# Performance work log

Hardware: AMD Instinct MI355X
Metric: run time of the kernel (lower is better)

Reference implementation:

```python
import jax, jax.numpy as jnp
import numpy as np

B, C, F, J = 64, 16, 2048, 25
EMBED, CLASSES, NJ = 64, 5, 12
AFFECT = slice(0, 12)
UNAFFECT = slice(12, 24)


def setup_inputs() -> dict:
    key = jax.random.key(0)
    k0, k1, k2, k3 = jax.random.split(key, 4)
    features = jax.random.normal(k0, (B, C, F, J), dtype=jnp.float32)
    W1 = jax.random.normal(k1, (EMBED, C, NJ), dtype=jnp.float32) * 0.05
    b1 = jnp.zeros((EMBED,), jnp.float32)
    W2 = jax.random.normal(k2, (EMBED, C, NJ), dtype=jnp.float32) * 0.05
    b2 = jnp.zeros((EMBED,), jnp.float32)
    Wl = jax.random.normal(k3, (CLASSES, 16 * EMBED), dtype=jnp.float32) * 0.02
    bl = jnp.zeros((CLASSES,), jnp.float32)
    return {"features": features, "W1": W1, "b1": b1, "W2": W2, "b2": b2, "Wl": Wl, "bl": bl}


def _stat_features(x, proto):
    # x: [b, c, f, j]; single sort shared by min/max/quantiles/median
    f = x.shape[-2]
    xs = jnp.sort(x, axis=-2)

    def quant(p):
        # torch.quantile linear interpolation
        pos = p * (f - 1)
        lo = int(np.floor(pos)); hi = int(np.ceil(pos)); frac = np.float32(pos - lo)
        return xs[..., lo, :] * (1.0 - frac) + xs[..., hi, :] * frac

    s1 = xs[..., 0, :]                       # min
    s2 = xs[..., -1, :]                      # max
    s3 = quant(0.25)
    s4 = xs[..., (f - 1) // 2, :]            # torch.median: lower middle element
    s5 = quant(0.75)
    s6 = jnp.mean(x, axis=-2)
    s7 = jnp.std(x, axis=-2, ddof=1)         # torch.std unbiased
    s8 = s2 - s1
    z = (x - s6[..., None, :]) / s7[..., None, :]
    if proto:
        s9 = jnp.mean(z ** 3, axis=-2)       # skew
    else:
        s9 = jnp.mean(z ** 4, axis=-2) - 3.0  # excess kurtosis
    return jnp.stack([s2, s3, s4, s5, s6, s7, s8, s9], axis=-2)  # [b, c, 8, j]


def _fuse(stat, W, b):
    # Conv2d kernel (1, joints) == contraction over (c, j) per stat row
    out = jnp.einsum('bcsj,ecj->bes', stat, W) + b[None, :, None]
    return out.reshape(out.shape[0], -1)  # flatten (embed, stats) like torch.flatten


def reference(features, W1, b1, W2, b2, Wl, bl):
    affected = features[:, :, :, AFFECT]
    unaffected = features[:, :, :, UNAFFECT]
    stat_af = _stat_features(affected, proto=False)
    stat_ua = _stat_features(unaffected, proto=False)
    # attn=False path (STAT_VA block disabled)
    stat1 = _stat_features(unaffected + affected, proto=True)
    _ = _fuse(stat1, W1, b1)  # stat1 branch only feeds CL loss (get_cl_loss=False)
    stat2 = jnp.concatenate([stat_af, stat_ua], axis=-2)  # [b, c, 16, j]
    flat2 = _fuse(stat2, W2, b2)                          # [b, 16*embed]
    logits = flat2 @ Wl.T + bl
    return logits
```

## Files before the change

kernel.cpp:

```cpp
#include <hip/hip_runtime.h>
#include <hip/hip_bf16.h>
#include <math.h>


#define F_LEN 2048
#define JTOT 25
#define STATS_PER_BC 192
#define LP 2056

__device__ __forceinline__ int swz(int i) {
  return (i & ~31) | ((i + ((i >> 5) << 2)) & 31);
}

template <int PAT>
__device__ __forceinline__ float ds_swz(float v) {
  return __int_as_float(
      __builtin_amdgcn_ds_swizzle(__float_as_int(v), PAT));
}

template <int CTRL, int BANK>
__device__ __forceinline__ int upd_dpp(int old_, int src) {
  return __builtin_amdgcn_update_dpp(old_, src, CTRL, 0xF, BANK, false);
}

__device__ __forceinline__ float xpartner(float v, const int lm,
                                          const int addr32) {
  const int vi = __float_as_int(v);
  switch (lm) {
    case 1:  return __int_as_float(upd_dpp<0xB1, 0xF>(vi, vi));
    case 2:  return __int_as_float(upd_dpp<0x4E, 0xF>(vi, vi));
    case 4: {
      const int t1 = upd_dpp<0x104, 0x5>(vi, vi);
      const int t2 = upd_dpp<0x114, 0xA>(t1, vi);
      return __int_as_float(t2);
    }
    case 8:  return __int_as_float(upd_dpp<0x128, 0xF>(vi, vi));
    case 16: return ds_swz<0x401F>(v);
    default:
      return __int_as_float(
          __builtin_amdgcn_ds_bpermute(addr32, vi));
  }
}

__device__ __forceinline__ float wave_sum(float v, int addr32) {
  v += xpartner(v, 1, addr32);
  v += xpartner(v, 2, addr32);
  v += xpartner(v, 4, addr32);
  v += xpartner(v, 8, addr32);
  v += xpartner(v, 16, addr32);
  v += xpartner(v, 32, addr32);
  return v;
}

#define XSUB8(CTRL, a0, a1, a2, a3, a4, a5, a6, a7, FL)                       \
  do {                                                                        \
    float t0, t1, t2, t3, t4, t5, t6, t7;                                     \
    asm volatile(                                                             \
        "v_xor_b32 %0, %16, %0\n\t"                                           \
        "v_xor_b32 %1, %16, %1\n\t"                                           \
        "v_xor_b32 %2, %16, %2\n\t"                                           \
        "v_xor_b32 %3, %16, %3\n\t"                                           \
        "v_xor_b32 %4, %16, %4\n\t"                                           \
        "v_xor_b32 %5, %16, %5\n\t"                                           \
        "v_xor_b32 %6, %16, %6\n\t"                                           \
        "v_xor_b32 %7, %16, %7\n\t"                                           \
        "v_mov_b32_dpp %8, %0 " CTRL "\n\t"                                   \
        "v_mov_b32_dpp %9, %1 " CTRL "\n\t"                                   \
        "v_mov_b32_dpp %10, %2 " CTRL "\n\t"                                  \
        "v_mov_b32_dpp %11, %3 " CTRL "\n\t"                                  \
        "v_mov_b32_dpp %12, %4 " CTRL "\n\t"                                  \
        "v_mov_b32_dpp %13, %5 " CTRL "\n\t"                                  \
        "v_mov_b32_dpp %14, %6 " CTRL "\n\t"                                  \
        "v_mov_b32_dpp %15, %7 " CTRL "\n\t"                                  \
        "v_min_f32 %0, %0, -%8\n\t"                                           \
        "v_min_f32 %1, %1, -%9\n\t"                                           \
        "v_min_f32 %2, %2, -%10\n\t"                                          \
        "v_min_f32 %3, %3, -%11\n\t"                                          \
        "v_min_f32 %4, %4, -%12\n\t"                                          \
        "v_min_f32 %5, %5, -%13\n\t"                                          \
        "v_min_f32 %6, %6, -%14\n\t"                                          \
        "v_min_f32 %7, %7, -%15\n\t"                                          \
        : "+v"(a0), "+v"(a1), "+v"(a2), "+v"(a3), "+v"(a4), "+v"(a5),         \
          "+v"(a6), "+v"(a7), "=&v"(t0), "=&v"(t1), "=&v"(t2), "=&v"(t3),     \
          "=&v"(t4), "=&v"(t5), "=&v"(t6), "=&v"(t7)                          \
        : "v"(FL));                                                           \
  } while (0)

#define XSUB8_X4(a0, a1, a2, a3, a4, a5, a6, a7, FL)                          \
  do {                                                                        \
    float t0, t1, t2, t3, t4, t5, t6, t7;                                     \
    asm volatile(                                                             \
        "v_xor_b32 %0, %16, %0\n\t"                                           \
        "v_xor_b32 %1, %16, %1\n\t"                                           \
        "v_xor_b32 %2, %16, %2\n\t"                                           \
        "v_xor_b32 %3, %16, %3\n\t"                                           \
        "v_xor_b32 %4, %16, %4\n\t"                                           \
        "v_xor_b32 %5, %16, %5\n\t"                                           \
        "v_xor_b32 %6, %16, %6\n\t"                                           \
        "v_xor_b32 %7, %16, %7\n\t"                                           \
        "v_mov_b32_dpp %8, %0 row_shl:4 row_mask:0xf bank_mask:0x5\n\t"       \
        "v_mov_b32_dpp %9, %1 row_shl:4 row_mask:0xf bank_mask:0x5\n\t"       \
        "v_mov_b32_dpp %10, %2 row_shl:4 row_mask:0xf bank_mask:0x5\n\t"      \
        "v_mov_b32_dpp %11, %3 row_shl:4 row_mask:0xf bank_mask:0x5\n\t"      \
        "v_mov_b32_dpp %12, %4 row_shl:4 row_mask:0xf bank_mask:0x5\n\t"      \
        "v_mov_b32_dpp %13, %5 row_shl:4 row_mask:0xf bank_mask:0x5\n\t"      \
        "v_mov_b32_dpp %14, %6 row_shl:4 row_mask:0xf bank_mask:0x5\n\t"      \
        "v_mov_b32_dpp %15, %7 row_shl:4 row_mask:0xf bank_mask:0x5\n\t"      \
        "v_mov_b32_dpp %8, %0 row_shr:4 row_mask:0xf bank_mask:0xa\n\t"       \
        "v_mov_b32_dpp %9, %1 row_shr:4 row_mask:0xf bank_mask:0xa\n\t"       \
        "v_mov_b32_dpp %10, %2 row_shr:4 row_mask:0xf bank_mask:0xa\n\t"      \
        "v_mov_b32_dpp %11, %3 row_shr:4 row_mask:0xf bank_mask:0xa\n\t"      \
        "v_mov_b32_dpp %12, %4 row_shr:4 row_mask:0xf bank_mask:0xa\n\t"      \
        "v_mov_b32_dpp %13, %5 row_shr:4 row_mask:0xf bank_mask:0xa\n\t"      \
        "v_mov_b32_dpp %14, %6 row_shr:4 row_mask:0xf bank_mask:0xa\n\t"      \
        "v_mov_b32_dpp %15, %7 row_shr:4 row_mask:0xf bank_mask:0xa\n\t"      \
        "v_min_f32 %0, %0, -%8\n\t"                                           \
        "v_min_f32 %1, %1, -%9\n\t"                                           \
        "v_min_f32 %2, %2, -%10\n\t"                                          \
        "v_min_f32 %3, %3, -%11\n\t"                                          \
        "v_min_f32 %4, %4, -%12\n\t"                                          \
        "v_min_f32 %5, %5, -%13\n\t"                                          \
        "v_min_f32 %6, %6, -%14\n\t"                                          \
        "v_min_f32 %7, %7, -%15\n\t"                                          \
        : "+v"(a0), "+v"(a1), "+v"(a2), "+v"(a3), "+v"(a4), "+v"(a5),         \
          "+v"(a6), "+v"(a7), "=&v"(t0), "=&v"(t1), "=&v"(t2), "=&v"(t3),     \
          "=&v"(t4), "=&v"(t5), "=&v"(t6), "=&v"(t7)                          \
        : "v"(FL));                                                           \
  } while (0)

#define QP1 "quad_perm:[1,0,3,2] row_mask:0xf bank_mask:0xf"
#define QP2 "quad_perm:[2,3,0,1] row_mask:0xf bank_mask:0xf"
#define ROR8 "row_ror:8 row_mask:0xf bank_mask:0xf"

#define XSUB32(M, CTRL, X, FL)                                                \
  do {                                                                        \
    M(CTRL, X[0], X[1], X[2], X[3], X[4], X[5], X[6], X[7], FL);              \
    M(CTRL, X[8], X[9], X[10], X[11], X[12], X[13], X[14], X[15], FL);        \
    M(CTRL, X[16], X[17], X[18], X[19], X[20], X[21], X[22], X[23], FL);      \
    M(CTRL, X[24], X[25], X[26], X[27], X[28], X[29], X[30], X[31], FL);      \
  } while (0)

#define XSUB32_X4(X, FL)                                                      \
  do {                                                                        \
    XSUB8_X4(X[0], X[1], X[2], X[3], X[4], X[5], X[6], X[7], FL);             \
    XSUB8_X4(X[8], X[9], X[10], X[11], X[12], X[13], X[14], X[15], FL);       \
    XSUB8_X4(X[16], X[17], X[18], X[19], X[20], X[21], X[22], X[23], FL);     \
    XSUB8_X4(X[24], X[25], X[26], X[27], X[28], X[29], X[30], X[31], FL);     \
  } while (0)

__global__ __launch_bounds__(256) void stat_kernel(
    const float* __restrict__ Fp, float* __restrict__ stat2) {
  __shared__ float lds[4 * LP];
  const int g = blockIdx.x;
  const int xcd = g & 7;
  const int mm = g >> 3;
  const int bc = xcd * 128 + mm / 6;
  const int grp = mm % 6;
  const int t = threadIdx.x;
  const int w = t >> 6;
  const int lane = t & 63;
  const int addr32 = ((lane ^ 32) << 2);
  const int j0 = grp * 4;
  float* wlds = lds + w * LP;

  {
    const float* bbase = Fp + (size_t)bc * F_LEN * JTOT + j0;
    const int f0 = t >> 2, jj = t & 3;
    float* ldst = lds + jj * LP;
#pragma unroll
    for (int it = 0; it < 32; ++it) {
      const int f = it * 64 + f0;
      ldst[swz(f)] = bbase[(size_t)f * JTOT + jj];
    }
  }
  __syncthreads();

  float x[32];
  {
    const float4* src4 = (const float4*)wlds;
#pragma unroll
    for (int q = 0; q < 8; ++q) {
      float4 v = src4[lane * 8 + ((lane + q) & 7)];
      x[4 * q] = v.x; x[4 * q + 1] = v.y;
      x[4 * q + 2] = v.z; x[4 * q + 3] = v.w;
    }
  }

  float sum = 0.f;
#pragma unroll
  for (int e = 0; e < 32; ++e) sum += x[e];
  sum = wave_sum(sum, addr32);
  const float m = sum * (1.0f / 2048.0f);

  float c2 = 0.f, c4 = 0.f;
#pragma unroll
  for (int e = 0; e < 32; ++e) {
    float d = x[e] - m;
    float dd = d * d;
    c2 += dd;
    c4 += dd * dd;
  }
  c2 = wave_sum(c2, addr32);
  c4 = wave_sum(c4, addr32);
  const float var = c2 * (1.0f / 2047.0f);
  const float sd = sqrtf(var);
  const float kurt = (c4 * (1.0f / 2048.0f)) / (var * var) - 3.0f;

#pragma unroll
  for (int kp = 1; kp <= 4; ++kp) {
    const int k = 1 << kp;
#pragma unroll
    for (int jp = kp - 1; jp >= 0; --jp) {
      const int st = 1 << jp;
#pragma unroll
      for (int e = 0; e < 32; ++e) {
        if ((e & st) == 0) {
          const bool up = ((e & k) == 0);
          float a = x[e], b = x[e + st];
          float lo2 = fminf(a, b), hi2 = fmaxf(a, b);
          x[e] = up ? lo2 : hi2;
          x[e + st] = up ? hi2 : lo2;
        }
      }
    }
  }

  unsigned Fst = 0u;
#pragma unroll
  for (int kp = 5; kp <= 10; ++kp) {
    const unsigned d = ((lane >> (kp - 5)) & 1) ? 0x80000000u : 0u;
#pragma unroll
    for (int jp = kp - 1; jp >= 5; --jp) {
      const int lm = 1 << (jp - 5);
      const unsigned r = ((lane >> (jp - 5)) & 1) ? 0x80000000u : 0u;
      const unsigned tgt = d ^ r;
      const unsigned fl = tgt ^ Fst;
      Fst = tgt;
      if (lm == 16) {
#pragma unroll
        for (int e = 0; e < 32; ++e)
          x[e] = __uint_as_float(__float_as_uint(x[e]) ^ fl);
#pragma unroll
        for (int e = 0; e < 32; ++e) {
          float o = ds_swz<0x401F>(x[e]);
          x[e] = fminf(x[e], -o);
        }
      } else if (lm == 1) {
        XSUB32(XSUB8, QP1, x, fl);
      } else if (lm == 2) {
        XSUB32(XSUB8, QP2, x, fl);
      } else if (lm == 4) {
        XSUB32_X4(x, fl);
      } else {
        XSUB32(XSUB8, ROR8, x, fl);
      }
    }
    {
      const unsigned fl = d ^ Fst;
      Fst = d;
#pragma unroll
      for (int e = 0; e < 32; ++e)
        x[e] = __uint_as_float(__float_as_uint(x[e]) ^ fl);
    }
#pragma unroll
    for (int jp = (kp - 1 < 4 ? kp - 1 : 4); jp >= 0; --jp) {
      const int st = 1 << jp;
#pragma unroll
      for (int e = 0; e < 32; ++e) {
        if ((e & st) == 0) {
          float a = x[e], b = x[e + st];
          x[e] = fminf(a, b);
          x[e + st] = fmaxf(a, b);
        }
      }
    }
  }
#pragma unroll
  for (int e = 0; e < 32; ++e)
    x[e] = __uint_as_float(__float_as_uint(x[e]) ^ Fst);

  {
    float4* dst4 = (float4*)wlds;
#pragma unroll
    for (int q = 0; q < 8; ++q) {
      int wq = 8 * lane + ((q + lane) & 7);
      dst4[wq] = make_float4(x[4 * q], x[4 * q + 1], x[4 * q + 2], x[4 * q + 3]);
    }
  }

  const int kk = (lane == 0) ? 511
               : (lane == 1) ? 512
               : (lane == 2) ? 1023
               : (lane == 3) ? 1535 : 1536;
  const int mtot = kk + 1;
  int lo = mtot - 1024; if (lo < 0) lo = 0;
  int hi = (mtot < 1024) ? mtot : 1024;
  for (int it = 0; it < 11; ++it) {
    const bool act = lo < hi;
    const int s = (lo + hi) >> 1;
    const int sa = (s < 1023) ? s : 1023;
    float Av = wlds[swz(sa)];
    Av = (s < 1024) ? Av : INFINITY;
    int bidx = mtot - s - 1;
    bidx = bidx < 0 ? 0 : (bidx > 1023 ? 1023 : bidx);
    const float Bv = wlds[swz(2047 - bidx)];
    const bool gg = act && (Bv > Av);
    if (gg) lo = s + 1;
    else if (act) hi = s;
  }
  float val;
  {
    const int s = lo;
    const int ia = (s - 1 < 0) ? 0 : s - 1;
    const float fa = wlds[swz(ia)];
    const float fromA = (s > 0) ? fa : -INFINITY;
    const int bi = mtot - s - 1;
    const int ib = (bi < 0) ? 0 : bi;
    const float fb = wlds[swz(2047 - ib)];
    const float fromB = (bi >= 0) ? fb : -INFINITY;
    val = fmaxf(fromA, fromB);
  }

  const float a511  = __shfl(val, 0, 64);
  const float a512  = __shfl(val, 1, 64);
  const float amed  = __shfl(val, 2, 64);
  const float a1535 = __shfl(val, 3, 64);
  const float a1536 = __shfl(val, 4, 64);

  if (lane == 0) {
    const float mn = fminf(wlds[swz(0)], wlds[swz(2047)]);
    const float mx = fmaxf(wlds[swz(1023)], wlds[swz(1024)]);
    const float q25 = 0.25f * a511 + 0.75f * a512;
    const float q75 = 0.75f * a1535 + 0.25f * a1536;
    const int j = j0 + w;
    const int jj = (j < 12) ? j : j - 12;
    const int sb = (j < 12) ? 0 : 8;
    float st8[8] = {mx, q25, amed, q75, m, sd, mx - mn, kurt};
    float* o = stat2 + (bc * 16 + sb) * 12 + jj;
#pragma unroll
    for (int s2 = 0; s2 < 8; ++s2) o[s2 * 12] = st8[s2];
  }
}

__global__ __launch_bounds__(256) void prep_kernel(
    const float* __restrict__ W2, const float* __restrict__ b2,
    const float* __restrict__ Wl, const float* __restrict__ bl,
    float* __restrict__ M, float* __restrict__ C) {
  const int g = blockIdx.x;
  const int t = threadIdx.x;
  if (g < 60) {
    const int id = g * 256 + t;
    const int k = id / 3072;
    const int r = id % 3072;
    const int c = r / 192;
    const int s = (r % 192) / 12;
    const int j = r % 12;
    const float* wl = Wl + k * 1024 + s;
    const float* w2 = W2 + c * 12 + j;
    float acc = 0.f;
#pragma unroll 8
    for (int e = 0; e < 64; ++e) acc += wl[e * 16] * w2[e * 192];
    M[id] = acc;
  } else if (t < 64) {
    const int e = t;
    const int addr32 = ((e ^ 32) << 2);
    for (int k = 0; k < 5; ++k) {
      const float* wl = Wl + k * 1024 + e * 16;
      float rs = 0.f;
#pragma unroll
      for (int s = 0; s < 16; ++s) rs += wl[s];
      float v = wave_sum(rs * b2[e], addr32);
      if (e == 0) C[k] = v + bl[k];
    }
  }
}

__global__ __launch_bounds__(256) void logits_kernel(
    const float* __restrict__ stat2, const float* __restrict__ M,
    const float* __restrict__ C, float* __restrict__ out) {
  __shared__ float s_red[20];
  const int b = blockIdx.x;
  const int t = threadIdx.x;
  const int lane = t & 63;
  const int w = t >> 6;
  const int addr32 = ((lane ^ 32) << 2);

  float acc[5] = {0.f, 0.f, 0.f, 0.f, 0.f};
#pragma unroll
  for (int ii = 0; ii < 12; ++ii) {
    const int i = ii * 256 + t;
    const float s = stat2[b * 3072 + i];
#pragma unroll
    for (int k = 0; k < 5; ++k) acc[k] += s * M[k * 3072 + i];
  }
#pragma unroll
  for (int k = 0; k < 5; ++k) acc[k] = wave_sum(acc[k], addr32);
  if (lane == 0) {
#pragma unroll
    for (int k = 0; k < 5; ++k) s_red[w * 5 + k] = acc[k];
  }
  __syncthreads();
  if (t < 5)
    out[b * 5 + t] =
        s_red[t] + s_red[5 + t] + s_red[10 + t] + s_red[15 + t] + C[t];
}

extern "C" void kernel_launch(void* const* d_in, const int* in_sizes, int n_in,
                              void* d_out, int out_size, void* d_ws,
                              size_t ws_size, hipStream_t stream) {
  const float* Fp = (const float*)d_in[0];
  const float* W2 = (const float*)d_in[3];
  const float* b2 = (const float*)d_in[4];
  const float* Wl = (const float*)d_in[5];
  const float* bl = (const float*)d_in[6];
  float* out = (float*)d_out;

  float* stat2 = (float*)d_ws;
  float* M = stat2 + 196608;
  float* C = M + 15360;

  prep_kernel<<<61, 256, 0, stream>>>(W2, b2, Wl, bl, M, C);
  stat_kernel<<<6144, 256, 0, stream>>>(Fp, stat2);
  logits_kernel<<<64, 256, 0, stream>>>(stat2, M, C, out);
}
```

Measured before the change: 382.6 us.

## Replace final merge-path selection with full bitonic sort stage and halve LDS staging

The previous code sorted two 1024-element halves and then used a per-lane binary search (merge-path) through LDS to find the quantile order statistics. Now the bitonic network runs one more stage across the full wave, using ds_bpermute for the 32-lane exchange and inline-asm ds_swizzle for the 16-lane one, so every order statistic can be read directly with shuffles. Separately, the LDS staging buffer is halved: two columns are loaded, read into registers by waves 0-1, then overwritten with the next two columns for waves 2-3. The gain from smaller LDS and no search is paid for with an extra sort stage of cross-lane permutes, an extra global-load phase and two more barriers.

```diff
diff --git a/kernel.cpp b/kernel.cpp
--- a/kernel.cpp
+++ b/kernel.cpp
@@ -50,6 +50,19 @@
   v += xpartner(v, 16, addr32);
   v += xpartner(v, 32, addr32);
   return v;
+}
+
+__device__ __forceinline__ void read_x(const float* wlds, int lane,
+                                       float* x) {
+  const float4* src4 = (const float4*)wlds;
+#pragma unroll
+  for (int q = 0; q < 8; ++q) {
+    float4 v = src4[lane * 8 + ((lane + q) & 7)];
+    x[4 * q] = v.x;
+    x[4 * q + 1] = v.y;
+    x[4 * q + 2] = v.z;
+    x[4 * q + 3] = v.w;
+  }
 }
 
 #define XSUB8(CTRL, a0, a1, a2, a3, a4, a5, a6, a7, FL)                       \
@@ -128,6 +141,76 @@
         : "v"(FL));                                                           \
   } while (0)
 
+#define XSUB8_SWZ(a0, a1, a2, a3, a4, a5, a6, a7, FL)                         \
+  do {                                                                        \
+    float t0, t1, t2, t3, t4, t5, t6, t7;                                     \
+    asm volatile(                                                             \
+        "v_xor_b32 %0, %16, %0\n\t"                                           \
+        "v_xor_b32 %1, %16, %1\n\t"                                           \
+        "v_xor_b32 %2, %16, %2\n\t"                                           \
+        "v_xor_b32 %3, %16, %3\n\t"                                           \
+        "v_xor_b32 %4, %16, %4\n\t"                                           \
+        "v_xor_b32 %5, %16, %5\n\t"                                           \
+        "v_xor_b32 %6, %16, %6\n\t"                                           \
+        "v_xor_b32 %7, %16, %7\n\t"                                           \
+        "ds_swizzle_b32 %8, %0 offset:0x401F\n\t"                             \
+        "ds_swizzle_b32 %9, %1 offset:0x401F\n\t"                             \
+        "ds_swizzle_b32 %10, %2 offset:0x401F\n\t"                            \
+        "ds_swizzle_b32 %11, %3 offset:0x401F\n\t"                            \
+        "ds_swizzle_b32 %12, %4 offset:0x401F\n\t"                            \
+        "ds_swizzle_b32 %13, %5 offset:0x401F\n\t"                            \
+        "ds_swizzle_b32 %14, %6 offset:0x401F\n\t"                            \
+        "ds_swizzle_b32 %15, %7 offset:0x401F\n\t"                            \
+        "s_waitcnt lgkmcnt(0)\n\t"                                            \
+        "v_min_f32 %0, %0, -%8\n\t"                                           \
+        "v_min_f32 %1, %1, -%9\n\t"                                           \
+        "v_min_f32 %2, %2, -%10\n\t"                                          \
+        "v_min_f32 %3, %3, -%11\n\t"                                          \
+        "v_min_f32 %4, %4, -%12\n\t"                                          \
+        "v_min_f32 %5, %5, -%13\n\t"                                          \
+        "v_min_f32 %6, %6, -%14\n\t"                                          \
+        "v_min_f32 %7, %7, -%15\n\t"                                          \
+        : "+v"(a0), "+v"(a1), "+v"(a2), "+v"(a3), "+v"(a4), "+v"(a5),         \
+          "+v"(a6), "+v"(a7), "=&v"(t0), "=&v"(t1), "=&v"(t2), "=&v"(t3),     \
+          "=&v"(t4), "=&v"(t5), "=&v"(t6), "=&v"(t7)                          \
+        : "v"(FL));                                                           \
+  } while (0)
+
+#define XSUB8_BP(a0, a1, a2, a3, a4, a5, a6, a7, FL, AD)                      \
+  do {                                                                        \
+    float t0, t1, t2, t3, t4, t5, t6, t7;                                     \
+    asm volatile(                                                             \
+        "v_xor_b32 %0, %16, %0\n\t"                                           \
+        "v_xor_b32 %1, %16, %1\n\t"                                           \
+        "v_xor_b32 %2, %16, %2\n\t"                                           \
+        "v_xor_b32 %3, %16, %3\n\t"                                           \
+        "v_xor_b32 %4, %16, %4\n\t"                                           \
+        "v_xor_b32 %5, %16, %5\n\t"                                           \
+        "v_xor_b32 %6, %16, %6\n\t"                                           \
+        "v_xor_b32 %7, %16, %7\n\t"                                           \
+        "ds_bpermute_b32 %8, %17, %0\n\t"                                     \
+        "ds_bpermute_b32 %9, %17, %1\n\t"                                     \
+        "ds_bpermute_b32 %10, %17, %2\n\t"                                    \
+        "ds_bpermute_b32 %11, %17, %3\n\t"                                    \
+        "ds_bpermute_b32 %12, %17, %4\n\t"                                    \
+        "ds_bpermute_b32 %13, %17, %5\n\t"                                    \
+        "ds_bpermute_b32 %14, %17, %6\n\t"                                    \
+        "ds_bpermute_b32 %15, %17, %7\n\t"                                    \
+        "s_waitcnt lgkmcnt(0)\n\t"                                            \
+        "v_min_f32 %0, %0, -%8\n\t"                                           \
+        "v_min_f32 %1, %1, -%9\n\t"                                           \
+        "v_min_f32 %2, %2, -%10\n\t"                                          \
+        "v_min_f32 %3, %3, -%11\n\t"                                          \
+        "v_min_f32 %4, %4, -%12\n\t"                                          \
+        "v_min_f32 %5, %5, -%13\n\t"                                          \
+        "v_min_f32 %6, %6, -%14\n\t"                                          \
+        "v_min_f32 %7, %7, -%15\n\t"                                          \
+        : "+v"(a0), "+v"(a1), "+v"(a2), "+v"(a3), "+v"(a4), "+v"(a5),         \
+          "+v"(a6), "+v"(a7), "=&v"(t0), "=&v"(t1), "=&v"(t2), "=&v"(t3),     \
+          "=&v"(t4), "=&v"(t5), "=&v"(t6), "=&v"(t7)                          \
+        : "v"(FL), "v"(AD));                                                  \
+  } while (0)
+
 #define QP1 "quad_perm:[1,0,3,2] row_mask:0xf bank_mask:0xf"
 #define QP2 "quad_perm:[2,3,0,1] row_mask:0xf bank_mask:0xf"
 #define ROR8 "row_ror:8 row_mask:0xf bank_mask:0xf"
@@ -148,9 +231,25 @@
     XSUB8_X4(X[24], X[25], X[26], X[27], X[28], X[29], X[30], X[31], FL);     \
   } while (0)
 
+#define XSUB32_SWZ(X, FL)                                                     \
+  do {                                                                        \
+    XSUB8_SWZ(X[0], X[1], X[2], X[3], X[4], X[5], X[6], X[7], FL);            \
+    XSUB8_SWZ(X[8], X[9], X[10], X[11], X[12], X[13], X[14], X[15], FL);      \
+    XSUB8_SWZ(X[16], X[17], X[18], X[19], X[20], X[21], X[22], X[23], FL);    \
+    XSUB8_SWZ(X[24], X[25], X[26], X[27], X[28], X[29], X[30], X[31], FL);    \
+  } while (0)
+
+#define XSUB32_BP(X, FL, AD)                                                  \
+  do {                                                                        \
+    XSUB8_BP(X[0], X[1], X[2], X[3], X[4], X[5], X[6], X[7], FL, AD);         \
+    XSUB8_BP(X[8], X[9], X[10], X[11], X[12], X[13], X[14], X[15], FL, AD);   \
+    XSUB8_BP(X[16], X[17], X[18], X[19], X[20], X[21], X[22], X[23], FL, AD); \
+    XSUB8_BP(X[24], X[25], X[26], X[27], X[28], X[29], X[30], X[31], FL, AD); \
+  } while (0)
+
 __global__ __launch_bounds__(256) void stat_kernel(
     const float* __restrict__ Fp, float* __restrict__ stat2) {
-  __shared__ float lds[4 * LP];
+  __shared__ float lds[2 * LP];
   const int g = blockIdx.x;
   const int xcd = g & 7;
   const int mm = g >> 3;
@@ -161,30 +260,26 @@
   const int lane = t & 63;
   const int addr32 = ((lane ^ 32) << 2);
   const int j0 = grp * 4;
-  float* wlds = lds + w * LP;
-
-  {
-    const float* bbase = Fp + (size_t)bc * F_LEN * JTOT + j0;
-    const int f0 = t >> 2, jj = t & 3;
-    float* ldst = lds + jj * LP;
-#pragma unroll
-    for (int it = 0; it < 32; ++it) {
-      const int f = it * 64 + f0;
-      ldst[swz(f)] = bbase[(size_t)f * JTOT + jj];
-    }
+
+  const int f0 = t >> 1, jj = t & 1;
+  float* ldst = lds + jj * LP;
+  const float* bbase = Fp + (size_t)bc * F_LEN * JTOT + j0;
+#pragma unroll
+  for (int it = 0; it < 16; ++it) {
+    const int f = it * 128 + f0;
+    ldst[swz(f)] = bbase[(size_t)f * JTOT + jj];
   }
   __syncthreads();
-
   float x[32];
-  {
-    const float4* src4 = (const float4*)wlds;
-#pragma unroll
-    for (int q = 0; q < 8; ++q) {
-      float4 v = src4[lane * 8 + ((lane + q) & 7)];
-      x[4 * q] = v.x; x[4 * q + 1] = v.y;
-      x[4 * q + 2] = v.z; x[4 * q + 3] = v.w;
-    }
-  }
+  if (w < 2) read_x(lds + w * LP, lane, x);
+  __syncthreads();
+#pragma unroll
+  for (int it = 0; it < 16; ++it) {
+    const int f = it * 128 + f0;
+    ldst[swz(f)] = bbase[(size_t)f * JTOT + 2 + jj];
+  }
+  __syncthreads();
+  if (w >= 2) read_x(lds + (w - 2) * LP, lane, x);
 
   float sum = 0.f;
 #pragma unroll
@@ -227,7 +322,7 @@
 
   unsigned Fst = 0u;
 #pragma unroll
-  for (int kp = 5; kp <= 10; ++kp) {
+  for (int kp = 5; kp <= 11; ++kp) {
     const unsigned d = ((lane >> (kp - 5)) & 1) ? 0x80000000u : 0u;
 #pragma unroll
     for (int jp = kp - 1; jp >= 5; --jp) {
@@ -236,23 +331,18 @@
       const unsigned tgt = d ^ r;
       const unsigned fl = tgt ^ Fst;
       Fst = tgt;
-      if (lm == 16) {
-#pragma unroll
-        for (int e = 0; e < 32; ++e)
-          x[e] = __uint_as_float(__float_as_uint(x[e]) ^ fl);
-#pragma unroll
-        for (int e = 0; e < 32; ++e) {
-          float o = ds_swz<0x401F>(x[e]);
-          x[e] = fminf(x[e], -o);
-        }
-      } else if (lm == 1) {
+      if (lm == 1) {
         XSUB32(XSUB8, QP1, x, fl);
       } else if (lm == 2) {
         XSUB32(XSUB8, QP2, x, fl);
       } else if (lm == 4) {
         XSUB32_X4(x, fl);
+      } else if (lm == 8) {
+        XSUB32(XSUB8, ROR8, x, fl);
+      } else if (lm == 16) {
+        XSUB32_SWZ(x, fl);
       } else {
-        XSUB32(XSUB8, ROR8, x, fl);
+        XSUB32_BP(x, fl, addr32);
       }
     }
     {
@@ -263,7 +353,7 @@
         x[e] = __uint_as_float(__float_as_uint(x[e]) ^ fl);
     }
 #pragma unroll
-    for (int jp = (kp - 1 < 4 ? kp - 1 : 4); jp >= 0; --jp) {
+    for (int jp = 4; jp >= 0; --jp) {
       const int st = 1 << jp;
 #pragma unroll
       for (int e = 0; e < 32; ++e) {
@@ -275,68 +365,23 @@
       }
     }
   }
-#pragma unroll
-  for (int e = 0; e < 32; ++e)
-    x[e] = __uint_as_float(__float_as_uint(x[e]) ^ Fst);
-
-  {
-    float4* dst4 = (float4*)wlds;
-#pragma unroll
-    for (int q = 0; q < 8; ++q) {
-      int wq = 8 * lane + ((q + lane) & 7);
-      dst4[wq] = make_float4(x[4 * q], x[4 * q + 1], x[4 * q + 2], x[4 * q + 3]);
-    }
-  }
-
-  const int kk = (lane == 0) ? 511
-               : (lane == 1) ? 512
-               : (lane == 2) ? 1023
-               : (lane == 3) ? 1535 : 1536;
-  const int mtot = kk + 1;
-  int lo = mtot - 1024; if (lo < 0) lo = 0;
-  int hi = (mtot < 1024) ? mtot : 1024;
-  for (int it = 0; it < 11; ++it) {
-    const bool act = lo < hi;
-    const int s = (lo + hi) >> 1;
-    const int sa = (s < 1023) ? s : 1023;
-    float Av = wlds[swz(sa)];
-    Av = (s < 1024) ? Av : INFINITY;
-    int bidx = mtot - s - 1;
-    bidx = bidx < 0 ? 0 : (bidx > 1023 ? 1023 : bidx);
-    const float Bv = wlds[swz(2047 - bidx)];
-    const bool gg = act && (Bv > Av);
-    if (gg) lo = s + 1;
-    else if (act) hi = s;
-  }
-  float val;
-  {
-    const int s = lo;
-    const int ia = (s - 1 < 0) ? 0 : s - 1;
-    const float fa = wlds[swz(ia)];
-    const float fromA = (s > 0) ? fa : -INFINITY;
-    const int bi = mtot - s - 1;
-    const int ib = (bi < 0) ? 0 : bi;
-    const float fb = wlds[swz(2047 - ib)];
-    const float fromB = (bi >= 0) ? fb : -INFINITY;
-    val = fmaxf(fromA, fromB);
-  }
-
-  const float a511  = __shfl(val, 0, 64);
-  const float a512  = __shfl(val, 1, 64);
-  const float amed  = __shfl(val, 2, 64);
-  const float a1535 = __shfl(val, 3, 64);
-  const float a1536 = __shfl(val, 4, 64);
+
+  const float mn = __shfl(x[0], 0, 64);
+  const float a511 = __shfl(x[31], 15, 64);
+  const float a512 = __shfl(x[0], 16, 64);
+  const float amed = __shfl(x[31], 31, 64);
+  const float a1535 = __shfl(x[31], 47, 64);
+  const float a1536 = __shfl(x[0], 48, 64);
+  const float mx = __shfl(x[31], 63, 64);
 
   if (lane == 0) {
-    const float mn = fminf(wlds[swz(0)], wlds[swz(2047)]);
-    const float mx = fmaxf(wlds[swz(1023)], wlds[swz(1024)]);
     const float q25 = 0.25f * a511 + 0.75f * a512;
     const float q75 = 0.75f * a1535 + 0.25f * a1536;
     const int j = j0 + w;
-    const int jj = (j < 12) ? j : j - 12;
+    const int jj2 = (j < 12) ? j : j - 12;
     const int sb = (j < 12) ? 0 : 8;
     float st8[8] = {mx, q25, amed, q75, m, sd, mx - mn, kurt};
-    float* o = stat2 + (bc * 16 + sb) * 12 + jj;
+    float* o = stat2 + (bc * 16 + sb) * 12 + jj2;
 #pragma unroll
     for (int s2 = 0; s2 < 8; ++s2) o[s2 * 12] = st8[s2];
   }
```

After: 399.1 us. +4.3%, slower.
